# Optimization experiments

Measured on AMD Instinct MI355X. Metric: run time of the kernel, lower is better.

## Reference

```python
import jax, jax.numpy as jnp
import numpy as np

BOS_TAG_ID = 0
EOS_TAG_ID = 1
NB_FEATURES = 5_000_000
T, L, F_PER = 16384, 64, 14


def setup_inputs() -> dict:
    key = jax.random.key(0)
    k1, k2, k3 = jax.random.split(key, 3)
    feat_idx = jax.random.randint(k1, (T, L, F_PER), 0, NB_FEATURES, dtype=jnp.int64 if jax.config.jax_enable_x64 else jnp.int32)
    emission_weights = jax.random.normal(k2, (NB_FEATURES, 1), dtype=jnp.float32)
    transitions = jax.random.normal(k3, (L, L), dtype=jnp.float32)
    return {"feat_idx": feat_idx, "emission_weights": emission_weights, "transitions": transitions}


def _get_emissions(feat_idx, emission_weights):
    # sparse [L, F] one-hot-count matrix @ [F,1] == gather + sum over the 14 feature ids
    w = emission_weights[:, 0]
    return w[feat_idx].sum(-1)[None]  # [1, T, L]


def _viterbi(emissions, transitions):
    B, T_, L_ = emissions.shape
    alpha0 = transitions[BOS_TAG_ID][None, :] + emissions[:, 0]  # [B, L]

    def step(alpha, em_t):
        # scores[b, prev, cur] = em_t[b, cur] + transitions[prev, cur] + alpha[b, prev]
        scores = em_t[:, None, :] + transitions[None] + alpha[:, :, None]
        new_alpha = scores.max(axis=1)
        bp = scores.argmax(axis=1)  # [B, L]
        return new_alpha, bp

    em_rest = jnp.swapaxes(emissions[:, 1:], 0, 1)  # [T-1, B, L]
    alpha, bps = jax.lax.scan(step, alpha0, em_rest)
    end_scores = alpha + transitions[:, EOS_TAG_ID][None, :]
    max_final_scores = end_scores.max(axis=1)
    final_tags = end_scores.argmax(axis=1)  # [B]

    def back(tag, bp):
        prev = jnp.take_along_axis(bp, tag[:, None], axis=1)[:, 0]
        return prev, prev

    _, path_rest = jax.lax.scan(back, final_tags, bps, reverse=True)  # [T-1, B]
    path = jnp.concatenate([path_rest.T, final_tags[:, None]], axis=1)  # [B, T]
    return max_final_scores, path


def reference(feat_idx, emission_weights, transitions):
    emissions = _get_emissions(feat_idx, emission_weights)
    scores, path = _viterbi(emissions, transitions)
    return scores, path
```

## Files before the change

kernel.cpp:

```cpp
#include <hip/hip_runtime.h>

#define T_LEN  16384
#define LTAG   64
#define F_PER  14
#define CHUNK  8
#define NCHUNK (T_LEN / CHUNK)
#define BOS_ID 0
#define EOS_ID 1
#define NREG   6
#define REGSZ  833334
#define WARM   40
#define WB     72

typedef __attribute__((ext_vector_type(4))) int i4;

static constexpr size_t EM_OFF = 0;
static constexpr size_t BP_OFF = EM_OFF + (size_t)T_LEN * 64 * 4;
static constexpr size_t AE_OFF = BP_OFF + (size_t)T_LEN * 64;
static constexpr size_t PS_OFF = AE_OFF + 512;

__global__ __launch_bounds__(256) void k_emissions(
    const int* __restrict__ idx, const float* __restrict__ w, float* __restrict__ em)
{
    __shared__ int sIdx[256 * F_PER];
    const int tid = threadIdx.x;
    const int* g = idx + (size_t)blockIdx.x * (256 * F_PER);
    for (int x = tid * 4; x < 256 * F_PER; x += 1024)
        *(i4*)(sIdx + x) = __builtin_nontemporal_load((const i4*)(g + x));
    __syncthreads();
    int id[F_PER];
#pragma unroll
    for (int f = 0; f < F_PER; ++f) id[f] = sIdx[tid * F_PER + f];
    float sf[F_PER];
#pragma unroll
    for (int f = 0; f < F_PER; ++f) sf[f] = 0.f;
    for (int r = 0; r < NREG; ++r) {
        const int lo = r * REGSZ;
#pragma unroll
        for (int f = 0; f < F_PER; ++f)
            if ((unsigned)(id[f] - lo) < (unsigned)REGSZ) sf[f] += w[id[f]];
    }
    float s = 0.f;
#pragma unroll
    for (int f = 0; f < F_PER; f += 2) s += sf[f] + sf[f + 1];
    em[(size_t)blockIdx.x * 256 + tid] = s;
}

__global__ __launch_bounds__(64, 2) void k_phase3(
    const float* __restrict__ trans, const float* __restrict__ em,
    unsigned char* __restrict__ bp, float* __restrict__ aEnd)
{
    __shared__ __align__(16) float sa[64];
    const int c = blockIdx.x;
    const int tid = threadIdx.x;
    const int t0 = c * CHUNK;
    int nsteps = (T_LEN - 1) - t0; if (nsteps > CHUNK) nsteps = CHUNK;

    float tr_[64];
#pragma unroll
    for (int i = 0; i < 64; ++i) tr_[i] = trans[i * 64 + tid];
#pragma unroll
    for (int i = 0; i < 64; ++i) asm volatile("" : "+v"(tr_[i]));

    float a; int tw;
    if (t0 <= WARM) { tw = 0; a = tr_[BOS_ID] + em[tid]; }
    else            { tw = t0 - WARM; a = em[(size_t)tw * 64 + tid]; }

    #define EMROW(t) em[(size_t)((t) < T_LEN - 1 ? (t) : T_LEN - 1) * 64 + tid]
    float p0 = EMROW(tw + 1), p1 = EMROW(tw + 2), p2 = EMROW(tw + 3), p3 = EMROW(tw + 4);
    const float4* ap = (const float4*)sa;

    for (int t = tw + 1; t <= t0; ++t) {
        const float e = p0;
        p0 = p1; p1 = p2; p2 = p3; p3 = EMROW(t + 4);
        sa[tid] = a;
        float m = -3.0e38f;
#pragma unroll
        for (int g = 0; g < 4; ++g) {
            const float4 v0 = ap[4*g+0], v1 = ap[4*g+1], v2 = ap[4*g+2], v3 = ap[4*g+3];
            float s0[16];
            s0[0]  = tr_[16*g+0]  + v0.x;  s0[1]  = tr_[16*g+1]  + v0.y;
            s0[2]  = tr_[16*g+2]  + v0.z;  s0[3]  = tr_[16*g+3]  + v0.w;
            s0[4]  = tr_[16*g+4]  + v1.x;  s0[5]  = tr_[16*g+5]  + v1.y;
            s0[6]  = tr_[16*g+6]  + v1.z;  s0[7]  = tr_[16*g+7]  + v1.w;
            s0[8]  = tr_[16*g+8]  + v2.x;  s0[9]  = tr_[16*g+9]  + v2.y;
            s0[10] = tr_[16*g+10] + v2.z;  s0[11] = tr_[16*g+11] + v2.w;
            s0[12] = tr_[16*g+12] + v3.x;  s0[13] = tr_[16*g+13] + v3.y;
            s0[14] = tr_[16*g+14] + v3.z;  s0[15] = tr_[16*g+15] + v3.w;
#pragma unroll
            for (int st = 8; st >= 1; st >>= 1)
#pragma unroll
                for (int i = 0; i < st; ++i) s0[i] = fmaxf(s0[i], s0[i + st]);
            m = fmaxf(m, s0[0]);
        }
        a = e + m;
    }

    const int tend = t0 + nsteps;
    for (int t = t0 + 1; t <= tend; ++t) {
        const float e = p0;
        p0 = p1; p1 = p2; p2 = p3; p3 = EMROW(t + 4);
        sa[tid] = a;
        float m = -3.0e38f; int bi = 0;
#pragma unroll
        for (int g = 0; g < 4; ++g) {
            const float4 v0 = ap[4*g+0], v1 = ap[4*g+1], v2 = ap[4*g+2], v3 = ap[4*g+3];
            float s0[16];
            s0[0]  = tr_[16*g+0]  + v0.x;  s0[1]  = tr_[16*g+1]  + v0.y;
            s0[2]  = tr_[16*g+2]  + v0.z;  s0[3]  = tr_[16*g+3]  + v0.w;
            s0[4]  = tr_[16*g+4]  + v1.x;  s0[5]  = tr_[16*g+5]  + v1.y;
            s0[6]  = tr_[16*g+6]  + v1.z;  s0[7]  = tr_[16*g+7]  + v1.w;
            s0[8]  = tr_[16*g+8]  + v2.x;  s0[9]  = tr_[16*g+9]  + v2.y;
            s0[10] = tr_[16*g+10] + v2.z;  s0[11] = tr_[16*g+11] + v2.w;
            s0[12] = tr_[16*g+12] + v3.x;  s0[13] = tr_[16*g+13] + v3.y;
            s0[14] = tr_[16*g+14] + v3.z;  s0[15] = tr_[16*g+15] + v3.w;
            float t16[16];
#pragma unroll
            for (int i = 0; i < 16; ++i) t16[i] = s0[i];
#pragma unroll
            for (int st = 8; st >= 1; st >>= 1)
#pragma unroll
                for (int i = 0; i < st; ++i) t16[i] = fmaxf(t16[i], t16[i + st]);
            const float gm = t16[0];
            int gb = 15;
#pragma unroll
            for (int i = 14; i >= 0; --i) gb = (s0[i] == gm) ? i : gb;
            if (gm > m) { m = gm; bi = 16*g + gb; }
        }
        a = e + m;
        bp[(size_t)t * 64 + tid] = (unsigned char)bi;
    }
    if (c == NCHUNK - 1) aEnd[tid] = a;
    #undef EMROW
}

__global__ __launch_bounds__(64) void k_backtrack(
    const float* __restrict__ trans, const float* __restrict__ em,
    const unsigned char* __restrict__ bp, const float* __restrict__ aEnd,
    float* __restrict__ out, double* __restrict__ partial)
{
    __shared__ __align__(16) unsigned char sbp[(CHUNK + WB) * 64];
    const int c = blockIdx.x;
    const int tid = threadIdx.x;
    const int t0 = c * CHUNK;
    int nsteps = (T_LEN - 1) - t0; if (nsteps > CHUNK) nsteps = CHUNK;
    int t_hi = t0 + nsteps + WB; if (t_hi > T_LEN - 1) t_hi = T_LEN - 1;
    const int nrows = t_hi - t0;

    const unsigned char* gsrc = bp + (size_t)(t0 + 1) * 64;
    for (int x = tid * 16; x < nrows * 64; x += 1024)
        *(i4*)(sbp + x) = *(const i4*)(gsrc + x);

    float val = aEnd[tid] + trans[tid * 64 + EOS_ID];
    int idx = tid;
#pragma unroll
    for (int o = 32; o >= 1; o >>= 1) {
        float ov = __shfl_xor(val, o);
        int   oi = __shfl_xor(idx, o);
        if (ov > val || (ov == val && oi < idx)) { val = ov; idx = oi; }
    }
    __syncthreads();

    int tag = (t_hi == T_LEN - 1) ? idx : 0;
    int pp = 0, pt = 0;
    for (int t = t_hi; t > t0; --t) {
        const int r = t - t0;
        if (tid == r)     pp = tag;
        if (tid + 1 == r) pt = tag;
        tag = sbp[(r - 1) * 64 + tag];
    }
    if (tid == 0) pp = tag;

    if (tid < nsteps) out[1 + t0 + tid] = (float)pp;
    if (c == NCHUNK - 1 && tid == nsteps) out[1 + (T_LEN - 1)] = (float)pp;

    double term = 0.0;
    if (tid < nsteps) {
        const int t = t0 + 1 + tid;
        term = (double)trans[pp * 64 + pt] + (double)em[(size_t)t * 64 + pt];
    }
    if (c == 0 && tid == 0)
        term += (double)trans[BOS_ID * 64 + pp] + (double)em[pp];
    if (c == NCHUNK - 1 && tid == nsteps)
        term += (double)trans[pp * 64 + EOS_ID];
#pragma unroll
    for (int o = 1; o < 64; o <<= 1) term += __shfl_xor(term, o);
    if (tid == 0) partial[c] = term;
}

__global__ __launch_bounds__(64) void k_sfin(
    const double* __restrict__ partial, float* __restrict__ out)
{
    const int tid = threadIdx.x;
    double s = 0.0;
    for (int k = tid; k < NCHUNK; k += 64) s += partial[k];
#pragma unroll
    for (int o = 1; o < 64; o <<= 1) s += __shfl_xor(s, o);
    if (tid == 0) out[0] = (float)s;
}

extern "C" void kernel_launch(void* const* d_in, const int* in_sizes, int n_in,
                              void* d_out, int out_size, void* d_ws, size_t ws_size,
                              hipStream_t stream)
{
    const int*   feat = (const int*)d_in[0];
    const float* w    = (const float*)d_in[1];
    const float* tr   = (const float*)d_in[2];
    float* out = (float*)d_out;
    char*  ws  = (char*)d_ws;

    float*         em = (float*)(ws + EM_OFF);
    unsigned char* bp = (unsigned char*)(ws + BP_OFF);
    float*         ae = (float*)(ws + AE_OFF);
    double*        ps = (double*)(ws + PS_OFF);

    k_emissions <<<(T_LEN * LTAG) / 256, 256, 0, stream>>>(feat, w, em);
    k_phase3    <<<NCHUNK, 64, 0, stream>>>(tr, em, bp, ae);
    k_backtrack <<<NCHUNK, 64, 0, stream>>>(tr, em, bp, ae, out, ps);
    k_sfin      <<<1,      64, 0, stream>>>(ps, out);
}
```

Measured before the change: 226.2 us.

## Fuse Viterbi forward, backtrack and score reduction into one kernel per chunk

```diff
diff --git a/kernel.cpp b/kernel.cpp
--- a/kernel.cpp
+++ b/kernel.cpp
@@ -3,7 +3,7 @@
 #define T_LEN  16384
 #define LTAG   64
 #define F_PER  14
-#define CHUNK  8
+#define CHUNK  16
 #define NCHUNK (T_LEN / CHUNK)
 #define BOS_ID 0
 #define EOS_ID 1
@@ -11,19 +11,19 @@
 #define REGSZ  833334
 #define WARM   40
 #define WB     72
+#define ROWS_MAX (WARM + CHUNK + WB + 1)
 
 typedef __attribute__((ext_vector_type(4))) int i4;
 
 static constexpr size_t EM_OFF = 0;
-static constexpr size_t BP_OFF = EM_OFF + (size_t)T_LEN * 64 * 4;
-static constexpr size_t AE_OFF = BP_OFF + (size_t)T_LEN * 64;
-static constexpr size_t PS_OFF = AE_OFF + 512;
 
 __global__ __launch_bounds__(256) void k_emissions(
-    const int* __restrict__ idx, const float* __restrict__ w, float* __restrict__ em)
+    const int* __restrict__ idx, const float* __restrict__ w, float* __restrict__ em,
+    float* __restrict__ out)
 {
     __shared__ int sIdx[256 * F_PER];
     const int tid = threadIdx.x;
+    if (blockIdx.x == 0 && tid == 0) out[0] = 0.f;
     const int* g = idx + (size_t)blockIdx.x * (256 * F_PER);
     for (int x = tid * 4; x < 256 * F_PER; x += 1024)
         *(i4*)(sIdx + x) = __builtin_nontemporal_load((const i4*)(g + x));
@@ -46,34 +46,39 @@
     em[(size_t)blockIdx.x * 256 + tid] = s;
 }
 
-__global__ __launch_bounds__(64, 2) void k_phase3(
+__global__ __launch_bounds__(64, 1) void k_viterbi(
     const float* __restrict__ trans, const float* __restrict__ em,
-    unsigned char* __restrict__ bp, float* __restrict__ aEnd)
+    float* __restrict__ out)
 {
+    __shared__ __align__(16) float sem[ROWS_MAX * 64];
+    __shared__ __align__(16) unsigned char sbp[(CHUNK + WB) * 64];
     __shared__ __align__(16) float sa[64];
     const int c = blockIdx.x;
     const int tid = threadIdx.x;
     const int t0 = c * CHUNK;
     int nsteps = (T_LEN - 1) - t0; if (nsteps > CHUNK) nsteps = CHUNK;
+    int t_hi = t0 + nsteps + WB; if (t_hi > T_LEN - 1) t_hi = T_LEN - 1;
+    const int tw = (t0 <= WARM) ? 0 : t0 - WARM;
+    const int nrows = t_hi - tw + 1;
+
+    const float* esrc = em + (size_t)tw * 64;
+    for (int x = tid * 4; x < nrows * 64; x += 256)
+        *(float4*)(sem + x) = *(const float4*)(esrc + x);
 
     float tr_[64];
 #pragma unroll
     for (int i = 0; i < 64; ++i) tr_[i] = trans[i * 64 + tid];
 #pragma unroll
     for (int i = 0; i < 64; ++i) asm volatile("" : "+v"(tr_[i]));
+    const float teos = trans[tid * 64 + EOS_ID];
+    __syncthreads();
 
-    float a; int tw;
-    if (t0 <= WARM) { tw = 0; a = tr_[BOS_ID] + em[tid]; }
-    else            { tw = t0 - WARM; a = em[(size_t)tw * 64 + tid]; }
-
-    #define EMROW(t) em[(size_t)((t) < T_LEN - 1 ? (t) : T_LEN - 1) * 64 + tid]
-    float p0 = EMROW(tw + 1), p1 = EMROW(tw + 2), p2 = EMROW(tw + 3), p3 = EMROW(tw + 4);
+    float a = (t0 <= WARM) ? (tr_[BOS_ID] + sem[tid]) : sem[tid];
     const float4* ap = (const float4*)sa;
 
     for (int t = tw + 1; t <= t0; ++t) {
-        const float e = p0;
-        p0 = p1; p1 = p2; p2 = p3; p3 = EMROW(t + 4);
         sa[tid] = a;
+        const float e = sem[(t - tw) * 64 + tid];
         float m = -3.0e38f;
 #pragma unroll
         for (int g = 0; g < 4; ++g) {
@@ -96,11 +101,9 @@
         a = e + m;
     }
 
-    const int tend = t0 + nsteps;
-    for (int t = t0 + 1; t <= tend; ++t) {
-        const float e = p0;
-        p0 = p1; p1 = p2; p2 = p3; p3 = EMROW(t + 4);
+    for (int t = t0 + 1; t <= t_hi; ++t) {
         sa[tid] = a;
+        const float e = sem[(t - tw) * 64 + tid];
         float m = -3.0e38f; int bi = 0;
 #pragma unroll
         for (int g = 0; g < 4; ++g) {
@@ -128,41 +131,23 @@
             if (gm > m) { m = gm; bi = 16*g + gb; }
         }
         a = e + m;
-        bp[(size_t)t * 64 + tid] = (unsigned char)bi;
+        sbp[(t - t0 - 1) * 64 + tid] = (unsigned char)bi;
     }
-    if (c == NCHUNK - 1) aEnd[tid] = a;
-    #undef EMROW
-}
 
-__global__ __launch_bounds__(64) void k_backtrack(
-    const float* __restrict__ trans, const float* __restrict__ em,
-    const unsigned char* __restrict__ bp, const float* __restrict__ aEnd,
-    float* __restrict__ out, double* __restrict__ partial)
-{
-    __shared__ __align__(16) unsigned char sbp[(CHUNK + WB) * 64];
-    const int c = blockIdx.x;
-    const int tid = threadIdx.x;
-    const int t0 = c * CHUNK;
-    int nsteps = (T_LEN - 1) - t0; if (nsteps > CHUNK) nsteps = CHUNK;
-    int t_hi = t0 + nsteps + WB; if (t_hi > T_LEN - 1) t_hi = T_LEN - 1;
-    const int nrows = t_hi - t0;
+    int start_tag = 0;
+    if (t_hi == T_LEN - 1) {
+        float val = a + teos;
+        int idx = tid;
+#pragma unroll
+        for (int o = 32; o >= 1; o >>= 1) {
+            float ov = __shfl_xor(val, o);
+            int   oi = __shfl_xor(idx, o);
+            if (ov > val || (ov == val && oi < idx)) { val = ov; idx = oi; }
+        }
+        start_tag = idx;
+    }
 
-    const unsigned char* gsrc = bp + (size_t)(t0 + 1) * 64;
-    for (int x = tid * 16; x < nrows * 64; x += 1024)
-        *(i4*)(sbp + x) = *(const i4*)(gsrc + x);
-
-    float val = aEnd[tid] + trans[tid * 64 + EOS_ID];
-    int idx = tid;
-#pragma unroll
-    for (int o = 32; o >= 1; o >>= 1) {
-        float ov = __shfl_xor(val, o);
-        int   oi = __shfl_xor(idx, o);
-        if (ov > val || (ov == val && oi < idx)) { val = ov; idx = oi; }
-    }
-    __syncthreads();
-
-    int tag = (t_hi == T_LEN - 1) ? idx : 0;
-    int pp = 0, pt = 0;
+    int tag = start_tag, pp = 0, pt = 0;
     for (int t = t_hi; t > t0; --t) {
         const int r = t - t0;
         if (tid == r)     pp = tag;
@@ -177,26 +162,15 @@
     double term = 0.0;
     if (tid < nsteps) {
         const int t = t0 + 1 + tid;
-        term = (double)trans[pp * 64 + pt] + (double)em[(size_t)t * 64 + pt];
+        term = (double)trans[pp * 64 + pt] + (double)sem[(t - tw) * 64 + pt];
     }
     if (c == 0 && tid == 0)
-        term += (double)trans[BOS_ID * 64 + pp] + (double)em[pp];
+        term += (double)trans[BOS_ID * 64 + pp] + (double)sem[pp];
     if (c == NCHUNK - 1 && tid == nsteps)
         term += (double)trans[pp * 64 + EOS_ID];
 #pragma unroll
     for (int o = 1; o < 64; o <<= 1) term += __shfl_xor(term, o);
-    if (tid == 0) partial[c] = term;
-}
-
-__global__ __launch_bounds__(64) void k_sfin(
-    const double* __restrict__ partial, float* __restrict__ out)
-{
-    const int tid = threadIdx.x;
-    double s = 0.0;
-    for (int k = tid; k < NCHUNK; k += 64) s += partial[k];
-#pragma unroll
-    for (int o = 1; o < 64; o <<= 1) s += __shfl_xor(s, o);
-    if (tid == 0) out[0] = (float)s;
+    if (tid == 0) atomicAdd(out, (float)term);
 }
 
 extern "C" void kernel_launch(void* const* d_in, const int* in_sizes, int n_in,
@@ -209,13 +183,8 @@
     float* out = (float*)d_out;
     char*  ws  = (char*)d_ws;
 
-    float*         em = (float*)(ws + EM_OFF);
-    unsigned char* bp = (unsigned char*)(ws + BP_OFF);
-    float*         ae = (float*)(ws + AE_OFF);
-    double*        ps = (double*)(ws + PS_OFF);
+    float* em = (float*)(ws + EM_OFF);
 
-    k_emissions <<<(T_LEN * LTAG) / 256, 256, 0, stream>>>(feat, w, em);
-    k_phase3    <<<NCHUNK, 64, 0, stream>>>(tr, em, bp, ae);
-    k_backtrack <<<NCHUNK, 64, 0, stream>>>(tr, em, bp, ae, out, ps);
-    k_sfin      <<<1,      64, 0, stream>>>(ps, out);
+    k_emissions <<<(T_LEN * LTAG) / 256, 256, 0, stream>>>(feat, w, em, out);
+    k_viterbi   <<<NCHUNK, 64, 0, stream>>>(tr, em, out);
 }
```

After: 286.4 us. +26.6%, slower.
